# Performance work log

Measured on AMD Instinct MI355X. Metric: run time of the kernel, lower is better.

Reference implementation:

```python
import jax, jax.numpy as jnp
import numpy as np

B, T = 64, 500
NUM_CONCEPT, DIM, SIZE_MEM = 1024, 64, 50


def setup_inputs() -> dict:
    key = jax.random.key(0)
    ks = jax.random.split(key, 16)
    d = DIM

    def lin(k, fin, fout):
        k1, k2 = jax.random.split(k)
        s = 1.0 / np.sqrt(fin)
        return (jax.random.uniform(k1, (fin, fout), jnp.float32, -s, s),
                jax.random.uniform(k2, (fout,), jnp.float32, -s, s))

    Wf, bf = lin(ks[4], 2 * d, d)
    We, be = lin(ks[5], d, d)
    Wa, ba = lin(ks[6], d, d)
    Wab, bab = lin(ks[7], d, 1)
    Wd, bd = lin(ks[8], d, 1)
    return {
        'concept_seq': jax.random.randint(ks[0], (B, T), 0, NUM_CONCEPT),
        'correct_seq': jax.random.randint(ks[1], (B, T), 0, 2),
        'num_concept': NUM_CONCEPT,
        'embed_key': jax.random.normal(ks[2], (NUM_CONCEPT, d), jnp.float32),
        'embed_value': jax.random.normal(ks[3], (2 * NUM_CONCEPT, d), jnp.float32),
        'Mk': jax.random.normal(ks[9], (SIZE_MEM, d), jnp.float32) * np.sqrt(2.0 / d),
        'Mv0': jax.random.normal(ks[10], (SIZE_MEM, d), jnp.float32) * np.sqrt(2.0 / d),
        'Wf': Wf, 'bf': bf, 'We': We, 'be': be, 'Wa': Wa, 'ba': ba,
        'Wab': Wab, 'bab': bab, 'Wd': Wd, 'bd': bd,
    }


def _forward(concept_seq, correct_seq, num_concept, embed_key, embed_value,
             Mk, Mv0, Wf, bf, We, be, Wa, ba, Wab, bab, Wd, bd):
    x = concept_seq + num_concept * correct_seq          # [B,T]
    k = embed_key[concept_seq]                           # [B,T,d]
    v = embed_value[x]                                   # [B,T,d]
    w = jax.nn.softmax(jnp.einsum('btd,sd->bts', k, Mk), axis=-1)  # [B,T,S]
    e = jax.nn.sigmoid(v @ We + be)                      # [B,T,d]
    a = jnp.tanh(v @ Wa + ba)                            # [B,T,d]

    bsz = concept_seq.shape[0]
    Mv_init = jnp.broadcast_to(Mv0, (bsz,) + Mv0.shape)  # [B,S,d]

    def step(Mvt, inp):
        wt, et, at = inp                                 # [B,S],[B,d],[B,d]
        u = wt[:, :, None]
        Mv_new = Mvt * (1.0 - u * et[:, None, :]) + u * at[:, None, :]
        return Mv_new, Mvt                               # emit pre-update state

    wT = jnp.swapaxes(w, 0, 1)                           # [T,B,S]
    eT = jnp.swapaxes(e, 0, 1)
    aT = jnp.swapaxes(a, 0, 1)
    _, Mv_pre = jax.lax.scan(step, Mv_init, (wT, eT, aT))  # [T,B,S,d]

    r = jnp.einsum('tbs,tbsd->btd', wT, Mv_pre)          # read content [B,T,d]
    f = jnp.tanh(jnp.concatenate([r, k], axis=-1) @ Wf + bf)
    stu_ability = jnp.tanh(f @ Wab + bab)                # [B,T,1] (dropout = eval identity)
    que_diff = jnp.tanh(k @ Wd + bd)                     # [B,T,1]
    return jax.nn.sigmoid(3.0 * stu_ability - que_diff)[..., 0]  # [B,T]


def reference(concept_seq, correct_seq, num_concept, embed_key, embed_value,
              Mk, Mv0, Wf, bf, We, be, Wa, ba, Wab, bab, Wd, bd):
    return _forward(concept_seq, correct_seq, num_concept, embed_key, embed_value,
                    Mk, Mv0, Wf, bf, We, be, Wa, ba, Wab, bab, Wd, bd)
```

## Files before the change

kernel.cpp:

```cpp
#include <hip/hip_runtime.h>
#include <hip/hip_bf16.h>
#include <math.h>

#define BB 64
#define TT 500
#define DD 64
#define SS 50
#define CH 20
#define NCH (TT / CH)

__device__ __forceinline__ float sigmoidf_(float x) { return 1.0f / (1.0f + __expf(-x)); }

__global__ __launch_bounds__(64) void k1_tables(
    const float* __restrict__ embed_key,
    const float* __restrict__ embed_value,
    const float* __restrict__ Mk,
    const float* __restrict__ We, const float* __restrict__ be,
    const float* __restrict__ Wa, const float* __restrict__ ba,
    int ncon, int nv,
    float* __restrict__ wTab, float* __restrict__ eTab, float* __restrict__ aTab)
{
    const int lane = threadIdx.x;
    if ((int)blockIdx.x < ncon) {
        const int c = blockIdx.x;
        __shared__ float mkS[SS][DD + 1];
        __shared__ float kS[DD];
        kS[lane] = embed_key[c * DD + lane];
        for (int s = 0; s < SS; ++s)
            mkS[s][lane] = Mk[s * DD + lane];
        __syncthreads();

        float sc = -1e30f;
        if (lane < SS) {
            float acc = 0.f;
            #pragma unroll
            for (int dd = 0; dd < DD; ++dd)
                acc = fmaf(kS[dd], mkS[lane][dd], acc);
            sc = acc;
        }
        float m = sc;
        #pragma unroll
        for (int off = 32; off >= 1; off >>= 1)
            m = fmaxf(m, __shfl_xor(m, off));
        float ex = (lane < SS) ? __expf(sc - m) : 0.f;
        float ssum = ex;
        #pragma unroll
        for (int off = 32; off >= 1; off >>= 1)
            ssum += __shfl_xor(ssum, off);
        if (lane < SS)
            wTab[c * SS + lane] = ex / ssum;
    } else {
        const int x = blockIdx.x - ncon;
        __shared__ float vS[DD];
        vS[lane] = embed_value[x * DD + lane];
        __syncthreads();
        float acc_e = be[lane];
        float acc_a = ba[lane];
        #pragma unroll
        for (int i = 0; i < DD; ++i) {
            const float vi = vS[i];
            acc_e = fmaf(vi, We[i * DD + lane], acc_e);
            acc_a = fmaf(vi, Wa[i * DD + lane], acc_a);
        }
        eTab[x * DD + lane] = sigmoidf_(acc_e);
        aTab[x * DD + lane] = tanhf(acc_a);
    }
}

#define STAGE_LOAD(T0)                                                       \
    {                                                                        \
        _Pragma("unroll")                                                    \
        for (int kk = 0; kk < 5; ++kk) {                                     \
            const int idx = lane + 64 * kk;                                  \
            const int tt = idx >> 4, j = idx & 15;                           \
            const int s = st + j;                                            \
            wr[kk] = (s < en) ? wTab[cL[(T0) + tt] * SS + s] : 0.f;          \
        }                                                                    \
        _Pragma("unroll")                                                    \
        for (int tt = 0; tt < CH; ++tt) {                                    \
            const int xx = xL[(T0) + tt];                                    \
            er[tt] = eTab[xx * DD + lane];                                   \
            ar[tt] = aTab[xx * DD + lane];                                   \
        }                                                                    \
    }

#define STAGE_WRITE()                                                        \
    {                                                                        \
        _Pragma("unroll")                                                    \
        for (int kk = 0; kk < 5; ++kk) wL[lane + 64 * kk] = wr[kk];          \
        _Pragma("unroll")                                                    \
        for (int tt = 0; tt < CH; ++tt) {                                    \
            eL[tt * DD + lane] = er[tt];                                     \
            aL[tt * DD + lane] = ar[tt];                                     \
        }                                                                    \
    }

#define UPD(WW, JJ)                                                          \
    {                                                                        \
        const float mv_ = Mv[JJ];                                            \
        if ((JJ) & 1) r1 = fmaf(WW, mv_, r1); else r0 = fmaf(WW, mv_, r0);   \
        Mv[JJ] = fmaf(-(WW), fmaf(e_, mv_, -a_), mv_);                       \
    }

__global__ __launch_bounds__(64) void k2_scan(
    const int* __restrict__ cseq,
    const int* __restrict__ corr,
    const int* __restrict__ ncp,
    const float* __restrict__ wTab,
    const float* __restrict__ eTab,
    const float* __restrict__ aTab,
    const float* __restrict__ Mv0,
    float* __restrict__ rOut)
{
    const int b = blockIdx.x >> 2;
    const int sgB = blockIdx.x & 3;
    const int lane = threadIdx.x;
    const int nc = ncp[0];

    __shared__ int xL[TT];
    __shared__ int cL[TT];
    __shared__ float __align__(16) wL[CH * 16];
    __shared__ float eL[CH * DD];
    __shared__ float aL[CH * DD];

    for (int i = lane; i < TT; i += 64) {
        const int c = cseq[b * TT + i];
        cL[i] = c;
        xL[i] = c + nc * corr[b * TT + i];
    }
    __syncthreads();

    const int st = (SS * sgB) >> 2;
    const int en = (SS * (sgB + 1)) >> 2;

    float Mv[13];
    #pragma unroll
    for (int j = 0; j < 13; ++j) {
        const int s = st + j;
        Mv[j] = (s < en) ? Mv0[s * DD + lane] : 0.f;
    }

    float wr[5], er[CH], ar[CH];

    STAGE_LOAD(0)
    STAGE_WRITE()
    __syncthreads();

    for (int ch = 0; ch < NCH; ++ch) {
        if (ch + 1 < NCH) STAGE_LOAD((ch + 1) * CH)

        #pragma unroll
        for (int tc = 0; tc < CH; ++tc) {
            const float4 w0 = *(const float4*)&wL[tc * 16 + 0];
            const float4 w1 = *(const float4*)&wL[tc * 16 + 4];
            const float4 w2 = *(const float4*)&wL[tc * 16 + 8];
            const float4 w3 = *(const float4*)&wL[tc * 16 + 12];
            const float e_ = eL[tc * DD + lane];
            const float a_ = aL[tc * DD + lane];
            float r0 = 0.f, r1 = 0.f;
            UPD(w0.x, 0)  UPD(w0.y, 1)  UPD(w0.z, 2)  UPD(w0.w, 3)
            UPD(w1.x, 4)  UPD(w1.y, 5)  UPD(w1.z, 6)  UPD(w1.w, 7)
            UPD(w2.x, 8)  UPD(w2.y, 9)  UPD(w2.z, 10) UPD(w2.w, 11)
            UPD(w3.x, 12)
            atomicAdd(&rOut[(size_t)(b * TT + ch * CH + tc) * DD + lane], r0 + r1);
        }
        __syncthreads();
        if (ch + 1 < NCH) STAGE_WRITE()
        __syncthreads();
    }
}

__global__ __launch_bounds__(256) void k3_output(
    const int* __restrict__ cseq,
    const float* __restrict__ embed_key,
    const float* __restrict__ rBuf,
    const float* __restrict__ Wf, const float* __restrict__ bf,
    const float* __restrict__ Wab, const float* __restrict__ bab,
    const float* __restrict__ Wd, const float* __restrict__ bd,
    float* __restrict__ out)
{
    const int tid = threadIdx.x;
    const int tx = tid & 15, ty = tid >> 4;
    const int bt0 = blockIdx.x * 64;

    __shared__ float __align__(16) wfS[128][64];
    __shared__ float __align__(16) catT[128][68];
    __shared__ float qS[64];
    __shared__ float redS[64][17];

    #pragma unroll
    for (int k = 0; k < 8; ++k) {
        const int idx = tid + k * 256;
        ((float4*)wfS)[idx] = ((const float4*)Wf)[idx];
    }

    {
        const int d = tid & 63;
        const int g = tid >> 6;
        const float wd = Wd[d];
        #pragma unroll
        for (int m = 0; m < 16; ++m) {
            const int btl = g + 4 * m;
            const int bt = bt0 + btl;
            const int c = cseq[bt];
            const float r  = rBuf[(size_t)bt * DD + d];
            const float kv = embed_key[c * DD + d];
            catT[d][btl] = r;
            catT[64 + d][btl] = kv;
            float q = kv * wd;
            #pragma unroll
            for (int off = 32; off >= 1; off >>= 1)
                q += __shfl_xor(q, off);
            if (d == 0) qS[btl] = q;
        }
    }
    __syncthreads();

    float acc[4][4] = {{0.f}};
    #pragma unroll 8
    for (int i = 0; i < 128; ++i) {
        const float4 wf = *(const float4*)&wfS[i][tx * 4];
        const float4 ct = *(const float4*)&catT[i][ty * 4];
        acc[0][0] = fmaf(ct.x, wf.x, acc[0][0]);
        acc[0][1] = fmaf(ct.x, wf.y, acc[0][1]);
        acc[0][2] = fmaf(ct.x, wf.z, acc[0][2]);
        acc[0][3] = fmaf(ct.x, wf.w, acc[0][3]);
        acc[1][0] = fmaf(ct.y, wf.x, acc[1][0]);
        acc[1][1] = fmaf(ct.y, wf.y, acc[1][1]);
        acc[1][2] = fmaf(ct.y, wf.z, acc[1][2]);
        acc[1][3] = fmaf(ct.y, wf.w, acc[1][3]);
        acc[2][0] = fmaf(ct.z, wf.x, acc[2][0]);
        acc[2][1] = fmaf(ct.z, wf.y, acc[2][1]);
        acc[2][2] = fmaf(ct.z, wf.z, acc[2][2]);
        acc[2][3] = fmaf(ct.z, wf.w, acc[2][3]);
        acc[3][0] = fmaf(ct.w, wf.x, acc[3][0]);
        acc[3][1] = fmaf(ct.w, wf.y, acc[3][1]);
        acc[3][2] = fmaf(ct.w, wf.z, acc[3][2]);
        acc[3][3] = fmaf(ct.w, wf.w, acc[3][3]);
    }

    #pragma unroll
    for (int ii = 0; ii < 4; ++ii) {
        float p = 0.f;
        #pragma unroll
        for (int jj = 0; jj < 4; ++jj) {
            const int j = tx * 4 + jj;
            const float f = tanhf(acc[ii][jj] + bf[j]);
            p = fmaf(f, Wab[j], p);
        }
        redS[ty * 4 + ii][tx] = p;
    }
    __syncthreads();

    if (tid < 64) {
        const int btl = tid;
        float s = 0.f;
        #pragma unroll
        for (int t2 = 0; t2 < 16; ++t2)
            s += redS[btl][t2];
        const float stu  = tanhf(s + bab[0]);
        const float diff = tanhf(qS[btl] + bd[0]);
        out[bt0 + btl] = sigmoidf_(3.0f * stu - diff);
    }
}

extern "C" void kernel_launch(void* const* d_in, const int* in_sizes, int n_in,
                              void* d_out, int out_size, void* d_ws, size_t ws_size,
                              hipStream_t stream)
{
    const int*   concept_seq = (const int*)  d_in[0];
    const int*   correct_seq = (const int*)  d_in[1];
    const int*   num_concept = (const int*)  d_in[2];
    const float* embed_key   = (const float*)d_in[3];
    const float* embed_value = (const float*)d_in[4];
    const float* Mk          = (const float*)d_in[5];
    const float* Mv0         = (const float*)d_in[6];
    const float* Wf          = (const float*)d_in[7];
    const float* bf          = (const float*)d_in[8];
    const float* We          = (const float*)d_in[9];
    const float* be          = (const float*)d_in[10];
    const float* Wa          = (const float*)d_in[11];
    const float* ba          = (const float*)d_in[12];
    const float* Wab         = (const float*)d_in[13];
    const float* bab         = (const float*)d_in[14];
    const float* Wd          = (const float*)d_in[15];
    const float* bd          = (const float*)d_in[16];
    float* out = (float*)d_out;

    const int NCON = in_sizes[3] / DD;
    const int NV   = in_sizes[4] / DD;

    float* wTab = (float*)d_ws;
    float* eTab = wTab + (size_t)NCON * SS;
    float* aTab = eTab + (size_t)NV * DD;
    float* rBuf = aTab + (size_t)NV * DD;

    hipMemsetAsync(rBuf, 0, (size_t)BB * TT * DD * sizeof(float), stream);

    k1_tables<<<NCON + NV, 64, 0, stream>>>(
        embed_key, embed_value, Mk, We, be, Wa, ba,
        NCON, NV, wTab, eTab, aTab);

    k2_scan<<<BB * 4, 64, 0, stream>>>(
        concept_seq, correct_seq, num_concept,
        wTab, eTab, aTab, Mv0, rBuf);

    k3_output<<<(BB * TT) / 64, 256, 0, stream>>>(
        concept_seq, embed_key, rBuf,
        Wf, bf, Wab, bab, Wd, bd, out);
}
```

Measured before the change: 190.1 us.

## Register double-buffer scan inputs, shuffle weights, write per-group partials instead of atomics

```diff
diff --git a/kernel.cpp b/kernel.cpp
--- a/kernel.cpp
+++ b/kernel.cpp
@@ -67,42 +67,49 @@
     }
 }
 
-#define STAGE_LOAD(T0)                                                       \
-    {                                                                        \
-        _Pragma("unroll")                                                    \
-        for (int kk = 0; kk < 5; ++kk) {                                     \
-            const int idx = lane + 64 * kk;                                  \
-            const int tt = idx >> 4, j = idx & 15;                           \
-            const int s = st + j;                                            \
-            wr[kk] = (s < en) ? wTab[cL[(T0) + tt] * SS + s] : 0.f;          \
-        }                                                                    \
-        _Pragma("unroll")                                                    \
-        for (int tt = 0; tt < CH; ++tt) {                                    \
-            const int xx = xL[(T0) + tt];                                    \
-            er[tt] = eTab[xx * DD + lane];                                   \
-            ar[tt] = aTab[xx * DD + lane];                                   \
-        }                                                                    \
-    }
-
-#define STAGE_WRITE()                                                        \
-    {                                                                        \
-        _Pragma("unroll")                                                    \
-        for (int kk = 0; kk < 5; ++kk) wL[lane + 64 * kk] = wr[kk];          \
-        _Pragma("unroll")                                                    \
-        for (int tt = 0; tt < CH; ++tt) {                                    \
-            eL[tt * DD + lane] = er[tt];                                     \
-            aL[tt * DD + lane] = ar[tt];                                     \
-        }                                                                    \
-    }
-
-#define UPD(WW, JJ)                                                          \
-    {                                                                        \
-        const float mv_ = Mv[JJ];                                            \
-        if ((JJ) & 1) r1 = fmaf(WW, mv_, r1); else r0 = fmaf(WW, mv_, r0);   \
-        Mv[JJ] = fmaf(-(WW), fmaf(e_, mv_, -a_), mv_);                       \
-    }
-
-__global__ __launch_bounds__(64) void k2_scan(
+#define GW(WD, KK, T0) {                                                     \
+    const int idx_ = lane + 64 * (KK);                                       \
+    const int tt_ = idx_ >> 4, j_ = idx_ & 15;                               \
+    const int s_ = st + j_;                                                  \
+    WD = (s_ < en) ? wTab[cL[(T0) + tt_] * SS + s_] : 0.f; }
+
+#define GLOAD(P, T0)                                                         \
+    GW(w##P##0, 0, T0) GW(w##P##1, 1, T0) GW(w##P##2, 2, T0)                 \
+    GW(w##P##3, 3, T0) GW(w##P##4, 4, T0)                                    \
+    _Pragma("unroll")                                                        \
+    for (int tt = 0; tt < CH; ++tt) {                                        \
+        const int xx_ = xL[(T0) + tt];                                       \
+        e##P[tt] = eTab[xx_ * DD + lane];                                    \
+        a##P[tt] = aTab[xx_ * DD + lane]; }
+
+#define U1(JJ, WREG) {                                                       \
+    const float w_ = __shfl((WREG), q_ * 16 + (JJ));                         \
+    const float mv_ = Mv[JJ];                                                \
+    if ((JJ) & 1) r1 = fmaf(w_, mv_, r1); else r0 = fmaf(w_, mv_, r0);       \
+    Mv[JJ] = fmaf(-w_, fmaf(e_, mv_, -a_), mv_); }
+
+#define STEP(P, WREG, tc, T0) {                                              \
+    const float e_ = e##P[tc], a_ = a##P[tc];                                \
+    const int q_ = (tc) & 3;                                                 \
+    float r0 = 0.f, r1 = 0.f;                                                \
+    U1(0, WREG)  U1(1, WREG)  U1(2, WREG)  U1(3, WREG)                       \
+    U1(4, WREG)  U1(5, WREG)  U1(6, WREG)  U1(7, WREG)                       \
+    U1(8, WREG)  U1(9, WREG)  U1(10, WREG) U1(11, WREG) U1(12, WREG)         \
+    rp[(size_t)((T0) + (tc)) * DD] = r0 + r1; }
+
+#define CCOMP(P, T0)                                                         \
+    STEP(P, w##P##0, 0, T0)  STEP(P, w##P##0, 1, T0)                         \
+    STEP(P, w##P##0, 2, T0)  STEP(P, w##P##0, 3, T0)                         \
+    STEP(P, w##P##1, 4, T0)  STEP(P, w##P##1, 5, T0)                         \
+    STEP(P, w##P##1, 6, T0)  STEP(P, w##P##1, 7, T0)                         \
+    STEP(P, w##P##2, 8, T0)  STEP(P, w##P##2, 9, T0)                         \
+    STEP(P, w##P##2, 10, T0) STEP(P, w##P##2, 11, T0)                        \
+    STEP(P, w##P##3, 12, T0) STEP(P, w##P##3, 13, T0)                        \
+    STEP(P, w##P##3, 14, T0) STEP(P, w##P##3, 15, T0)                        \
+    STEP(P, w##P##4, 16, T0) STEP(P, w##P##4, 17, T0)                        \
+    STEP(P, w##P##4, 18, T0) STEP(P, w##P##4, 19, T0)
+
+__global__ __launch_bounds__(64, 1) void k2_scan(
     const int* __restrict__ cseq,
     const int* __restrict__ corr,
     const int* __restrict__ ncp,
@@ -110,7 +117,7 @@
     const float* __restrict__ eTab,
     const float* __restrict__ aTab,
     const float* __restrict__ Mv0,
-    float* __restrict__ rOut)
+    float* __restrict__ rPart)
 {
     const int b = blockIdx.x >> 2;
     const int sgB = blockIdx.x & 3;
@@ -119,10 +126,6 @@
 
     __shared__ int xL[TT];
     __shared__ int cL[TT];
-    __shared__ float __align__(16) wL[CH * 16];
-    __shared__ float eL[CH * DD];
-    __shared__ float aL[CH * DD];
-
     for (int i = lane; i < TT; i += 64) {
         const int c = cseq[b * TT + i];
         cL[i] = c;
@@ -140,40 +143,29 @@
         Mv[j] = (s < en) ? Mv0[s * DD + lane] : 0.f;
     }
 
-    float wr[5], er[CH], ar[CH];
-
-    STAGE_LOAD(0)
-    STAGE_WRITE()
-    __syncthreads();
-
-    for (int ch = 0; ch < NCH; ++ch) {
-        if (ch + 1 < NCH) STAGE_LOAD((ch + 1) * CH)
-
-        #pragma unroll
-        for (int tc = 0; tc < CH; ++tc) {
-            const float4 w0 = *(const float4*)&wL[tc * 16 + 0];
-            const float4 w1 = *(const float4*)&wL[tc * 16 + 4];
-            const float4 w2 = *(const float4*)&wL[tc * 16 + 8];
-            const float4 w3 = *(const float4*)&wL[tc * 16 + 12];
-            const float e_ = eL[tc * DD + lane];
-            const float a_ = aL[tc * DD + lane];
-            float r0 = 0.f, r1 = 0.f;
-            UPD(w0.x, 0)  UPD(w0.y, 1)  UPD(w0.z, 2)  UPD(w0.w, 3)
-            UPD(w1.x, 4)  UPD(w1.y, 5)  UPD(w1.z, 6)  UPD(w1.w, 7)
-            UPD(w2.x, 8)  UPD(w2.y, 9)  UPD(w2.z, 10) UPD(w2.w, 11)
-            UPD(w3.x, 12)
-            atomicAdd(&rOut[(size_t)(b * TT + ch * CH + tc) * DD + lane], r0 + r1);
-        }
-        __syncthreads();
-        if (ch + 1 < NCH) STAGE_WRITE()
-        __syncthreads();
-    }
+    float* rp = rPart + ((size_t)sgB * BB + b) * TT * DD + lane;
+
+    float eA[CH], aA[CH], eB[CH], aB[CH];
+    float wA0, wA1, wA2, wA3, wA4, wB0, wB1, wB2, wB3, wB4;
+
+    GLOAD(A, 0)
+
+    for (int ch = 0; ch < NCH - 1; ch += 2) {
+        const int T0a = ch * CH;
+        const int T0b = T0a + CH;
+        const int T0c = T0a + 2 * CH;
+        GLOAD(B, T0b)
+        CCOMP(A, T0a)
+        GLOAD(A, T0c)
+        CCOMP(B, T0b)
+    }
+    CCOMP(A, (NCH - 1) * CH)
 }
 
 __global__ __launch_bounds__(256) void k3_output(
     const int* __restrict__ cseq,
     const float* __restrict__ embed_key,
-    const float* __restrict__ rBuf,
+    const float* __restrict__ rPart,
     const float* __restrict__ Wf, const float* __restrict__ bf,
     const float* __restrict__ Wab, const float* __restrict__ bab,
     const float* __restrict__ Wd, const float* __restrict__ bd,
@@ -203,7 +195,11 @@
             const int btl = g + 4 * m;
             const int bt = bt0 + btl;
             const int c = cseq[bt];
-            const float r  = rBuf[(size_t)bt * DD + d];
+            const size_t o = (size_t)bt * DD + d;
+            const float r = rPart[o]
+                          + rPart[(size_t)1 * BB * TT * DD + o]
+                          + rPart[(size_t)2 * BB * TT * DD + o]
+                          + rPart[(size_t)3 * BB * TT * DD + o];
             const float kv = embed_key[c * DD + d];
             catT[d][btl] = r;
             catT[64 + d][btl] = kv;
@@ -290,12 +286,10 @@
     const int NCON = in_sizes[3] / DD;
     const int NV   = in_sizes[4] / DD;
 
-    float* wTab = (float*)d_ws;
-    float* eTab = wTab + (size_t)NCON * SS;
-    float* aTab = eTab + (size_t)NV * DD;
-    float* rBuf = aTab + (size_t)NV * DD;
-
-    hipMemsetAsync(rBuf, 0, (size_t)BB * TT * DD * sizeof(float), stream);
+    float* wTab  = (float*)d_ws;
+    float* eTab  = wTab + (size_t)NCON * SS;
+    float* aTab  = eTab + (size_t)NV * DD;
+    float* rPart = aTab + (size_t)NV * DD;
 
     k1_tables<<<NCON + NV, 64, 0, stream>>>(
         embed_key, embed_value, Mk, We, be, Wa, ba,
@@ -303,9 +297,9 @@
 
     k2_scan<<<BB * 4, 64, 0, stream>>>(
         concept_seq, correct_seq, num_concept,
-        wTab, eTab, aTab, Mv0, rBuf);
+        wTab, eTab, aTab, Mv0, rPart);
 
     k3_output<<<(BB * TT) / 64, 256, 0, stream>>>(
-        concept_seq, embed_key, rBuf,
+        concept_seq, embed_key, rPart,
         Wf, bf, Wab, bab, Wd, bd, out);
 }
```

Result: slower. 207.9 us (+9.4%).
